# Optimization experiments

Hardware: AMD Instinct MI355X
Metric: run time of the kernel (lower is better)

Reference implementation:

```python
import jax, jax.numpy as jnp
import numpy as np

B, S, D = 2, 2048, 1024  # batch, seq, model_dim
E, K, H = 8, 2, 4096     # experts, top_k, expert hidden
CAP_FACTOR = 1.0


def setup_inputs() -> dict:
    key = jax.random.key(0)
    ks = jax.random.split(key, 6)
    scale_in = 1.0 / np.sqrt(D)
    scale_h = 1.0 / np.sqrt(H)
    return {
        "x": jax.random.normal(ks[0], (B, S, D), jnp.float32),
        "wg": jax.random.normal(ks[1], (D, E), jnp.float32) * scale_in,
        "w1": jax.random.normal(ks[2], (E, D, H), jnp.float32) * scale_in,
        "b1": jnp.zeros((E, H), jnp.float32),
        "w2": jax.random.normal(ks[3], (E, H, D), jnp.float32) * scale_h,
        "b2": jnp.zeros((E, D), jnp.float32),
    }


def _moe_forward(x, wg, w1, b1, w2, b2):
    Bb, Ss, Dd = x.shape
    T = Bb * Ss
    cap = int(K * CAP_FACTOR * ((T + E - 1) // E))  # Tutel capacity rule
    xt = x.reshape(T, Dd)

    # ---- gating ----
    logits = xt @ wg                      # [T, E]
    scores = jax.nn.softmax(logits, axis=-1)
    gates_k, idx_k = jax.lax.top_k(scores, K)  # [T, K]
    # normalize_gate=True: renormalize top-k gates
    gates_k = gates_k / jnp.sum(gates_k, axis=-1, keepdims=True)

    # ---- GShard-style location assignment (slot-major cumsum) ----
    masks = jax.nn.one_hot(idx_k, E, dtype=jnp.int32)           # [T, K, E]
    m = jnp.transpose(masks, (1, 0, 2)).reshape(K * T, E)       # slot-major
    locs_full = jnp.cumsum(m, axis=0) - 1                       # [K*T, E]
    loc = jnp.sum(locs_full * m, axis=-1)                       # [K*T]
    loc = loc.reshape(K, T).T                                   # [T, K]
    valid = (loc < cap).astype(xt.dtype)                        # capacity drop
    loc_c = jnp.clip(loc, 0, cap - 1)

    # ---- dispatch: scatter tokens into [E, cap, D] ----
    contrib = (xt[:, None, :] * valid[:, :, None]).reshape(T * K, Dd)
    disp = jnp.zeros((E, cap, Dd), xt.dtype)
    disp = disp.at[idx_k.reshape(-1), loc_c.reshape(-1)].add(contrib)

    # ---- grouped expert FFN ----
    h = jax.nn.relu(jnp.einsum("ecd,edh->ech", disp, w1) + b1[:, None, :])
    out = jnp.einsum("ech,ehd->ecd", h, w2) + b2[:, None, :]

    # ---- combine (postscore): gather + gate-weighted sum ----
    gathered = out[idx_k, loc_c]                                # [T, K, D]
    y = jnp.einsum("tk,tkd->td", gates_k * valid, gathered)
    return y.reshape(Bb, Ss, Dd)


def reference(x, wg, w1, b1, w2, b2):
    return _moe_forward(x, wg, w1, b1, w2, b2)
```

## Files before the change

kernel.cpp:

```cpp
#include <hip/hip_runtime.h>
#include <stdint.h>

#define NTOK 4096
#define DIM  1024
#define NEXP 8
#define HID  4096
#define CAP  1024

typedef __bf16 bf16x8 __attribute__((ext_vector_type(8)));
typedef float  f32x4  __attribute__((ext_vector_type(4)));

__device__ __forceinline__ unsigned short f2bf(float f) {
  unsigned int u = __float_as_uint(f);
  return (unsigned short)((u + 0x7fffu + ((u >> 16) & 1u)) >> 16);
}

__device__ __forceinline__ float bf2f(unsigned int bits16) {
  return __uint_as_float(bits16 << 16);
}

__device__ __forceinline__ void load_lds16(const void* g, void* l) {
  __builtin_amdgcn_global_load_lds(
      (__attribute__((address_space(1))) void*)g,
      (__attribute__((address_space(3))) void*)l,
      16, 0, 0);
}

__global__ void gating_kernel(const float* __restrict__ x, const float* __restrict__ wg,
                              int* __restrict__ tok_e, float* __restrict__ tok_g) {
  const int t = blockIdx.x;
  const int l = threadIdx.x;
  float acc[NEXP];
#pragma unroll
  for (int e = 0; e < NEXP; ++e) acc[e] = 0.f;

  const float4* x4  = (const float4*)(x + (size_t)t * DIM);
  const float4* wg4 = (const float4*)wg;
#pragma unroll
  for (int i = 0; i < 4; ++i) {
    int dq = i * 64 + l;
    float4 xv = x4[dq];
    float xs[4] = {xv.x, xv.y, xv.z, xv.w};
#pragma unroll
    for (int c = 0; c < 4; ++c) {
      int d = dq * 4 + c;
      float4 wa = wg4[d * 2], wb = wg4[d * 2 + 1];
      acc[0] += xs[c] * wa.x; acc[1] += xs[c] * wa.y;
      acc[2] += xs[c] * wa.z; acc[3] += xs[c] * wa.w;
      acc[4] += xs[c] * wb.x; acc[5] += xs[c] * wb.y;
      acc[6] += xs[c] * wb.z; acc[7] += xs[c] * wb.w;
    }
  }
#pragma unroll
  for (int off = 32; off; off >>= 1)
#pragma unroll
    for (int e = 0; e < NEXP; ++e) acc[e] += __shfl_xor(acc[e], off);

  if (l == 0) {
    float m = acc[0];
#pragma unroll
    for (int e = 1; e < NEXP; ++e) m = fmaxf(m, acc[e]);
    float p[NEXP];
#pragma unroll
    for (int e = 0; e < NEXP; ++e) p[e] = __expf(acc[e] - m);
    int e0 = 0; float b0 = p[0];
#pragma unroll
    for (int e = 1; e < NEXP; ++e) if (p[e] > b0) { b0 = p[e]; e0 = e; }
    int e1 = -1; float b1v = -1.f;
#pragma unroll
    for (int e = 0; e < NEXP; ++e) if (e != e0 && p[e] > b1v) { b1v = p[e]; e1 = e; }
    float inv = 1.f / (b0 + b1v);
    tok_e[2 * t] = e0; tok_e[2 * t + 1] = e1;
    tok_g[2 * t] = b0 * inv; tok_g[2 * t + 1] = b1v * inv;
  }
}

__global__ void scan_kernel(const int* __restrict__ tok_e, int* __restrict__ tok_loc,
                            int* __restrict__ slot_map) {
  const int l = threadIdx.x;
  const unsigned long long below = (1ull << l) - 1ull;
  int base[NEXP];
#pragma unroll
  for (int e = 0; e < NEXP; ++e) base[e] = 0;

  int nxt = tok_e[((0 * 64 + l) & (NTOK - 1)) * 2 + ((0 * 64 + l) >> 12)];
  for (int it = 0; it < 128; ++it) {
    int e = nxt;
    if (it + 1 < 128) {
      int g2 = (it + 1) * 64 + l;
      nxt = tok_e[(g2 & (NTOK - 1)) * 2 + (g2 >> 12)];
    }
    int loc = 0;
#pragma unroll
    for (int ex = 0; ex < NEXP; ++ex) {
      unsigned long long msk = __ballot(e == ex);
      int off = __popcll(msk & below);
      if (e == ex) loc = base[ex] + off;
      base[ex] += __popcll(msk);
    }
    int g = it * 64 + l;
    int k = g >> 12, t = g & (NTOK - 1);
    bool valid = loc < CAP;
    tok_loc[t * 2 + k] = valid ? loc : -1;
    if (valid) slot_map[e * CAP + loc] = t;
  }
#pragma unroll
  for (int ex = 0; ex < NEXP; ++ex) {
    int c = base[ex] < CAP ? base[ex] : CAP;
    for (int i = c + l; i < CAP; i += 64) slot_map[ex * CAP + i] = -1;
  }
}

__global__ void dispatch_kernel(const float* __restrict__ x, const int* __restrict__ slot_map,
                                unsigned short* __restrict__ disp) {
  const int s = blockIdx.x;
  const int tid = threadIdx.x;
  int t = slot_map[s];
  uint2 o;
  if (t >= 0) {
    float4 v = ((const float4*)(x + (size_t)t * DIM))[tid];
    o.x = (unsigned)f2bf(v.x) | ((unsigned)f2bf(v.y) << 16);
    o.y = (unsigned)f2bf(v.z) | ((unsigned)f2bf(v.w) << 16);
  } else {
    o.x = 0u; o.y = 0u;
  }
  ((uint2*)(disp + (size_t)s * DIM))[tid] = o;
}

__global__ void transpose_cvt(const float* __restrict__ in, unsigned short* __restrict__ out,
                              int R, int C) {
  __shared__ float tile[128][65];
  const int e = blockIdx.z;
  const float* inp = in + (size_t)e * R * C;
  unsigned short* outp = out + (size_t)e * R * C;
  const int c0 = blockIdx.x * 64, r0 = blockIdx.y * 128;
  const int t = threadIdx.x;
#pragma unroll
  for (int i = 0; i < 8; ++i) {
    int idx = i * 256 + t;
    int r = idx >> 4, c4 = (idx & 15) * 4;
    float4 v = *(const float4*)(inp + (size_t)(r0 + r) * C + c0 + c4);
    tile[r][c4 + 0] = v.x; tile[r][c4 + 1] = v.y;
    tile[r][c4 + 2] = v.z; tile[r][c4 + 3] = v.w;
  }
  __syncthreads();
#pragma unroll
  for (int i = 0; i < 4; ++i) {
    int idx = i * 256 + t;
    int c = idx >> 4, r8 = (idx & 15) * 8;
    unsigned short s[8];
#pragma unroll
    for (int j = 0; j < 8; ++j) s[j] = f2bf(tile[r8 + j][c]);
    uint4 o;
    o.x = (unsigned)s[0] | ((unsigned)s[1] << 16);
    o.y = (unsigned)s[2] | ((unsigned)s[3] << 16);
    o.z = (unsigned)s[4] | ((unsigned)s[5] << 16);
    o.w = (unsigned)s[6] | ((unsigned)s[7] << 16);
    *(uint4*)(outp + (size_t)(c0 + c) * R + r0 + r8) = o;
  }
}

template <bool RELU>
__global__ __launch_bounds__(256, 4)
void gemm_kernel(const unsigned short* __restrict__ A, const unsigned short* __restrict__ B,
                 const float* __restrict__ bias, unsigned short* __restrict__ C,
                 int N, int K) {
  __shared__ __align__(16) unsigned short As[2][128 * 32];
  __shared__ __align__(16) unsigned short Bs[2][128 * 32];

  int bid = blockIdx.x;
  const int cpx = (int)gridDim.x >> 3;
  bid = (bid & 7) * cpx + (bid >> 3);
  const int ntn = N >> 7;
  const int per_e = 8 * ntn;
  const int e = bid / per_e;
  const int rb = bid - e * per_e;
  const int mtile = rb / ntn;
  const int ntile = rb - mtile * ntn;

  A += (size_t)e * 1024 * K;
  B += (size_t)e * N * K;
  bias += (size_t)e * N;
  C += (size_t)e * 1024 * N;
  const int m0 = mtile * 128;
  const int n0 = ntile * 128;

  const int tid = threadIdx.x;
  const int wave = tid >> 6, lane = tid & 63;
  const int wm = wave >> 1, wn = wave & 1;
  const int quad = lane >> 4;

  const int srow = lane >> 2;
  const int scol = ((lane & 3) ^ (srow & 3)) * 8;
  const unsigned short* gA = A + (size_t)(m0 + wave * 16 + srow) * K + scol;
  const unsigned short* gB = B + (size_t)(n0 + wave * 16 + srow) * K + scol;

  f32x4 acc[4][4] = {};

  const int coff = (quad ^ (lane & 3)) * 8;
  const int arowb = (wm * 64 + (lane & 15)) * 32;
  const int browb = (wn * 64 + (lane & 15)) * 32;

#pragma unroll
  for (int i = 0; i < 2; ++i) {
    load_lds16(gA + (size_t)i * 64 * K, &As[0][(i * 64 + wave * 16) * 32]);
    load_lds16(gB + (size_t)i * 64 * K, &Bs[0][(i * 64 + wave * 16) * 32]);
  }
  gA += 32; gB += 32;

  const int nIter = K >> 5;
  for (int t = 0; t < nIter; ++t) {
    const int cur = t & 1;
    __syncthreads();
    if (t + 1 < nIter) {
#pragma unroll
      for (int i = 0; i < 2; ++i) {
        load_lds16(gA + (size_t)i * 64 * K, &As[cur ^ 1][(i * 64 + wave * 16) * 32]);
        load_lds16(gB + (size_t)i * 64 * K, &Bs[cur ^ 1][(i * 64 + wave * 16) * 32]);
      }
      gA += 32; gB += 32;
    }
    bf16x8 af[4], bfr[4];
#pragma unroll
    for (int i = 0; i < 4; ++i)
      af[i] = *reinterpret_cast<const bf16x8*>(&As[cur][arowb + i * 512 + coff]);
#pragma unroll
    for (int j = 0; j < 4; ++j)
      bfr[j] = *reinterpret_cast<const bf16x8*>(&Bs[cur][browb + j * 512 + coff]);
#pragma unroll
    for (int i = 0; i < 4; ++i)
#pragma unroll
      for (int j = 0; j < 4; ++j)
        acc[i][j] = __builtin_amdgcn_mfma_f32_16x16x32_bf16(af[i], bfr[j], acc[i][j], 0, 0, 0);
  }

  __syncthreads();
  unsigned short* scr = (wave < 2 ? &As[0][0] : &Bs[0][0]) + (wave & 1) * 2304;
  const int lc = lane & 15;
  const int erow = lane >> 3;
  const int ecol = (lane & 7) * 8;
#pragma unroll
  for (int p = 0; p < 2; ++p) {
#pragma unroll
    for (int j = 0; j < 4; ++j) {
      float bj = bias[n0 + wn * 64 + j * 16 + lc];
#pragma unroll
      for (int ii = 0; ii < 2; ++ii) {
#pragma unroll
        for (int rr = 0; rr < 4; ++rr) {
          float v = acc[p * 2 + ii][j][rr] + bj;
          if (RELU) v = fmaxf(v, 0.f);
          scr[(ii * 16 + quad * 4 + rr) * 72 + j * 16 + lc] = f2bf(v);
        }
      }
    }
    __asm__ volatile("s_waitcnt lgkmcnt(0)" ::: "memory");
    unsigned short* Cbase = C + (size_t)(m0 + wm * 64 + p * 32) * N + n0 + wn * 64;
#pragma unroll
    for (int pp = 0; pp < 4; ++pp) {
      uint4 v = *(const uint4*)&scr[(pp * 8 + erow) * 72 + ecol];
      *(uint4*)&Cbase[(size_t)(pp * 8 + erow) * N + ecol] = v;
    }
  }
}

__global__ void combine_kernel(const unsigned short* __restrict__ outb,
                               const int* __restrict__ tok_e, const int* __restrict__ tok_loc,
                               const float* __restrict__ tok_g, float* __restrict__ y) {
  const int t = blockIdx.x;
  const int tid = threadIdx.x;
  int e0 = tok_e[2 * t], e1 = tok_e[2 * t + 1];
  int l0 = tok_loc[2 * t], l1 = tok_loc[2 * t + 1];
  float g0 = tok_g[2 * t], g1 = tok_g[2 * t + 1];
  float ax = 0.f, ay = 0.f, az = 0.f, aw = 0.f;
  if (l0 >= 0) {
    uint2 u = ((const uint2*)(outb + ((size_t)e0 * CAP + l0) * DIM))[tid];
    ax += g0 * bf2f(u.x & 0xffffu); ay += g0 * __uint_as_float(u.x & 0xffff0000u);
    az += g0 * bf2f(u.y & 0xffffu); aw += g0 * __uint_as_float(u.y & 0xffff0000u);
  }
  if (l1 >= 0) {
    uint2 u = ((const uint2*)(outb + ((size_t)e1 * CAP + l1) * DIM))[tid];
    ax += g1 * bf2f(u.x & 0xffffu); ay += g1 * __uint_as_float(u.x & 0xffff0000u);
    az += g1 * bf2f(u.y & 0xffffu); aw += g1 * __uint_as_float(u.y & 0xffff0000u);
  }
  float4 o; o.x = ax; o.y = ay; o.z = az; o.w = aw;
  ((float4*)(y + (size_t)t * DIM))[tid] = o;
}

extern "C" void kernel_launch(void* const* d_in, const int* in_sizes, int n_in,
                              void* d_out, int out_size, void* d_ws, size_t ws_size,
                              hipStream_t stream) {
  const float* x  = (const float*)d_in[0];
  const float* wg = (const float*)d_in[1];
  const float* w1 = (const float*)d_in[2];
  const float* b1 = (const float*)d_in[3];
  const float* w2 = (const float*)d_in[4];
  const float* b2 = (const float*)d_in[5];
  float* y = (float*)d_out;

  char* ws = (char*)d_ws;
  int*   tok_e    = (int*)(ws);
  int*   tok_loc  = (int*)(ws + 32768);
  float* tok_g    = (float*)(ws + 65536);
  int*   slot_map = (int*)(ws + 98304);
  unsigned short* disp = (unsigned short*)(ws + 131072);
  unsigned short* wbuf = (unsigned short*)(ws + 131072 + (16ull << 20));
  unsigned short* h    = (unsigned short*)(ws + 131072 + (80ull << 20));
  unsigned short* outb = (unsigned short*)(ws + 131072 + (144ull << 20));

  gating_kernel<<<NTOK, 64, 0, stream>>>(x, wg, tok_e, tok_g);
  scan_kernel<<<1, 64, 0, stream>>>(tok_e, tok_loc, slot_map);
  dispatch_kernel<<<NEXP * CAP, 256, 0, stream>>>(x, slot_map, disp);
  transpose_cvt<<<dim3(HID / 64, DIM / 128, NEXP), 256, 0, stream>>>(w1, wbuf, DIM, HID);
  gemm_kernel<true><<<NEXP * 8 * (HID / 128), 256, 0, stream>>>(disp, wbuf, b1, h, HID, DIM);
  transpose_cvt<<<dim3(DIM / 64, HID / 128, NEXP), 256, 0, stream>>>(w2, wbuf, HID, DIM);
  gemm_kernel<false><<<NEXP * 8 * (DIM / 128), 256, 0, stream>>>(h, wbuf, b2, outb, DIM, HID);
  combine_kernel<<<NTOK, 256, 0, stream>>>(outb, tok_e, tok_loc, tok_g, y);
}
```

Baseline: 559.2 us.

## Rewrite expert GEMM with 128x256 tiles, 3-stage LDS pipeline, 8 waves

Replaces the 128x128, double-buffered, 4-wave GEMM with a 128x256 tile using 8 waves, a K-step of 64, and a triple-buffered global_load_lds pipeline in 144KB of dynamic LDS. Loads are issued two stages ahead, with explicit vmcnt waits and raw s_barrier instead of __syncthreads. MFMAs run at raised priority. The aim is to hide global load latency and cut barrier and LDS traffic per MFMA. In exchange occupancy drops to one block per CU and the grid gets smaller, which risks tail imbalance, especially on the second GEMM with only 256 blocks.

```diff
diff --git a/kernel.cpp b/kernel.cpp
--- a/kernel.cpp
+++ b/kernel.cpp
@@ -161,17 +161,18 @@
 }
 
 template <bool RELU>
-__global__ __launch_bounds__(256, 4)
-void gemm_kernel(const unsigned short* __restrict__ A, const unsigned short* __restrict__ B,
-                 const float* __restrict__ bias, unsigned short* __restrict__ C,
-                 int N, int K) {
-  __shared__ __align__(16) unsigned short As[2][128 * 32];
-  __shared__ __align__(16) unsigned short Bs[2][128 * 32];
+__global__ __launch_bounds__(512, 1)
+void gemm3(const unsigned short* __restrict__ A, const unsigned short* __restrict__ B,
+           const float* __restrict__ bias, unsigned short* __restrict__ C,
+           int N, int K) {
+  extern __shared__ __align__(16) unsigned short smem[];
+  unsigned short* As = smem;
+  unsigned short* Bs = smem + 3 * 8192;
 
   int bid = blockIdx.x;
   const int cpx = (int)gridDim.x >> 3;
   bid = (bid & 7) * cpx + (bid >> 3);
-  const int ntn = N >> 7;
+  const int ntn = N >> 8;
   const int per_e = 8 * ntn;
   const int e = bid / per_e;
   const int rb = bid - e * per_e;
@@ -183,84 +184,102 @@
   bias += (size_t)e * N;
   C += (size_t)e * 1024 * N;
   const int m0 = mtile * 128;
-  const int n0 = ntile * 128;
+  const int n0 = ntile * 256;
 
   const int tid = threadIdx.x;
-  const int wave = tid >> 6, lane = tid & 63;
-  const int wm = wave >> 1, wn = wave & 1;
+  const int w = tid >> 6, lane = tid & 63;
+  const int wm = w >> 2, wn = w & 3;
   const int quad = lane >> 4;
-
-  const int srow = lane >> 2;
-  const int scol = ((lane & 3) ^ (srow & 3)) * 8;
-  const unsigned short* gA = A + (size_t)(m0 + wave * 16 + srow) * K + scol;
-  const unsigned short* gB = B + (size_t)(n0 + wave * 16 + srow) * K + scol;
+  const int l15 = lane & 15;
+
+  const int srow = lane >> 3;
+  const int scol = ((lane & 7) ^ srow) * 8;
+  const unsigned short* gA = A + (size_t)(m0 + w * 8 + srow) * K + scol;
+  const unsigned short* gB = B + (size_t)(n0 + w * 8 + srow) * K + scol;
+  const int lbase = w * 512;
+
+  int coff[2];
+  coff[0] = ((quad + 0) ^ (lane & 7)) * 8;
+  coff[1] = ((quad + 4) ^ (lane & 7)) * 8;
+  const int arow = (wm * 64 + l15) * 64;
+  const int brow = (wn * 64 + l15) * 64;
 
   f32x4 acc[4][4] = {};
-
-  const int coff = (quad ^ (lane & 3)) * 8;
-  const int arowb = (wm * 64 + (lane & 15)) * 32;
-  const int browb = (wn * 64 + (lane & 15)) * 32;
-
-#pragma unroll
-  for (int i = 0; i < 2; ++i) {
-    load_lds16(gA + (size_t)i * 64 * K, &As[0][(i * 64 + wave * 16) * 32]);
-    load_lds16(gB + (size_t)i * 64 * K, &Bs[0][(i * 64 + wave * 16) * 32]);
-  }
-  gA += 32; gB += 32;
-
-  const int nIter = K >> 5;
-  for (int t = 0; t < nIter; ++t) {
-    const int cur = t & 1;
-    __syncthreads();
-    if (t + 1 < nIter) {
-#pragma unroll
-      for (int i = 0; i < 2; ++i) {
-        load_lds16(gA + (size_t)i * 64 * K, &As[cur ^ 1][(i * 64 + wave * 16) * 32]);
-        load_lds16(gB + (size_t)i * 64 * K, &Bs[cur ^ 1][(i * 64 + wave * 16) * 32]);
+  const int nt = K >> 6;
+
+#define STAGE(T, BUF)                                                           \
+  { _Pragma("unroll")                                                           \
+    for (int q_ = 0; q_ < 2; ++q_)                                              \
+      load_lds16(gA + (size_t)(q_ * 64) * K + (size_t)(T) * 64,                 \
+                 &As[(BUF) * 8192 + lbase + q_ * 4096]);                        \
+    _Pragma("unroll")                                                           \
+    for (int q_ = 0; q_ < 4; ++q_)                                              \
+      load_lds16(gB + (size_t)(q_ * 64) * K + (size_t)(T) * 64,                 \
+                 &Bs[(BUF) * 16384 + lbase + q_ * 4096]); }
+
+  STAGE(0, 0);
+  STAGE(1, 1);
+  asm volatile("s_waitcnt vmcnt(6)" ::: "memory");
+  __builtin_amdgcn_s_barrier();
+  __builtin_amdgcn_sched_barrier(0);
+
+  int cur = 0;
+  for (int t = 0; t < nt; ++t) {
+    const bool s2 = (t + 2) < nt;
+    if (s2) {
+      int nx2 = cur - 1; if (nx2 < 0) nx2 = 2;
+      STAGE(t + 2, nx2);
+    }
+    bf16x8 af[4][2], bfr[4][2];
+#pragma unroll
+    for (int f = 0; f < 4; ++f)
+#pragma unroll
+      for (int kk = 0; kk < 2; ++kk)
+        af[f][kk] = *(const bf16x8*)&As[cur * 8192 + arow + f * 1024 + coff[kk]];
+#pragma unroll
+    for (int j = 0; j < 4; ++j)
+#pragma unroll
+      for (int kk = 0; kk < 2; ++kk)
+        bfr[j][kk] = *(const bf16x8*)&Bs[cur * 16384 + brow + j * 1024 + coff[kk]];
+    __builtin_amdgcn_s_setprio(1);
+#pragma unroll
+    for (int kk = 0; kk < 2; ++kk)
+#pragma unroll
+      for (int i = 0; i < 4; ++i)
+#pragma unroll
+        for (int j = 0; j < 4; ++j)
+          acc[i][j] = __builtin_amdgcn_mfma_f32_16x16x32_bf16(af[i][kk], bfr[j][kk],
+                                                              acc[i][j], 0, 0, 0);
+    __builtin_amdgcn_s_setprio(0);
+    if (s2) { asm volatile("s_waitcnt vmcnt(6)" ::: "memory"); }
+    else    { asm volatile("s_waitcnt vmcnt(0)" ::: "memory"); }
+    __builtin_amdgcn_s_barrier();
+    __builtin_amdgcn_sched_barrier(0);
+    ++cur; if (cur == 3) cur = 0;
+  }
+#undef STAGE
+
+  unsigned short* scr = smem + w * 4608;
+#pragma unroll
+  for (int j = 0; j < 4; ++j) {
+    float bj = bias[n0 + wn * 64 + j * 16 + l15];
+#pragma unroll
+    for (int i = 0; i < 4; ++i)
+#pragma unroll
+      for (int rr = 0; rr < 4; ++rr) {
+        float v = acc[i][j][rr] + bj;
+        if (RELU) v = fmaxf(v, 0.f);
+        scr[(i * 16 + quad * 4 + rr) * 72 + j * 16 + l15] = f2bf(v);
       }
-      gA += 32; gB += 32;
-    }
-    bf16x8 af[4], bfr[4];
-#pragma unroll
-    for (int i = 0; i < 4; ++i)
-      af[i] = *reinterpret_cast<const bf16x8*>(&As[cur][arowb + i * 512 + coff]);
-#pragma unroll
-    for (int j = 0; j < 4; ++j)
-      bfr[j] = *reinterpret_cast<const bf16x8*>(&Bs[cur][browb + j * 512 + coff]);
-#pragma unroll
-    for (int i = 0; i < 4; ++i)
-#pragma unroll
-      for (int j = 0; j < 4; ++j)
-        acc[i][j] = __builtin_amdgcn_mfma_f32_16x16x32_bf16(af[i], bfr[j], acc[i][j], 0, 0, 0);
-  }
-
-  __syncthreads();
-  unsigned short* scr = (wave < 2 ? &As[0][0] : &Bs[0][0]) + (wave & 1) * 2304;
-  const int lc = lane & 15;
+  }
+  __asm__ volatile("s_waitcnt lgkmcnt(0)" ::: "memory");
   const int erow = lane >> 3;
   const int ecol = (lane & 7) * 8;
-#pragma unroll
-  for (int p = 0; p < 2; ++p) {
-#pragma unroll
-    for (int j = 0; j < 4; ++j) {
-      float bj = bias[n0 + wn * 64 + j * 16 + lc];
-#pragma unroll
-      for (int ii = 0; ii < 2; ++ii) {
-#pragma unroll
-        for (int rr = 0; rr < 4; ++rr) {
-          float v = acc[p * 2 + ii][j][rr] + bj;
-          if (RELU) v = fmaxf(v, 0.f);
-          scr[(ii * 16 + quad * 4 + rr) * 72 + j * 16 + lc] = f2bf(v);
-        }
-      }
-    }
-    __asm__ volatile("s_waitcnt lgkmcnt(0)" ::: "memory");
-    unsigned short* Cbase = C + (size_t)(m0 + wm * 64 + p * 32) * N + n0 + wn * 64;
-#pragma unroll
-    for (int pp = 0; pp < 4; ++pp) {
-      uint4 v = *(const uint4*)&scr[(pp * 8 + erow) * 72 + ecol];
-      *(uint4*)&Cbase[(size_t)(pp * 8 + erow) * N + ecol] = v;
-    }
+  unsigned short* Cbase = C + (size_t)(m0 + wm * 64) * N + n0 + wn * 64;
+#pragma unroll
+  for (int p = 0; p < 8; ++p) {
+    uint4 v = *(const uint4*)&scr[(p * 8 + erow) * 72 + ecol];
+    *(uint4*)&Cbase[(size_t)(p * 8 + erow) * N + ecol] = v;
   }
 }
 
@@ -308,12 +327,21 @@
   unsigned short* h    = (unsigned short*)(ws + 131072 + (80ull << 20));
   unsigned short* outb = (unsigned short*)(ws + 131072 + (144ull << 20));
 
+  static int att = 0;
+  if (!att) {
+    (void)hipFuncSetAttribute(reinterpret_cast<const void*>(&gemm3<true>),
+                              hipFuncAttributeMaxDynamicSharedMemorySize, 147456);
+    (void)hipFuncSetAttribute(reinterpret_cast<const void*>(&gemm3<false>),
+                              hipFuncAttributeMaxDynamicSharedMemorySize, 147456);
+    att = 1;
+  }
+
   gating_kernel<<<NTOK, 64, 0, stream>>>(x, wg, tok_e, tok_g);
   scan_kernel<<<1, 64, 0, stream>>>(tok_e, tok_loc, slot_map);
   dispatch_kernel<<<NEXP * CAP, 256, 0, stream>>>(x, slot_map, disp);
   transpose_cvt<<<dim3(HID / 64, DIM / 128, NEXP), 256, 0, stream>>>(w1, wbuf, DIM, HID);
-  gemm_kernel<true><<<NEXP * 8 * (HID / 128), 256, 0, stream>>>(disp, wbuf, b1, h, HID, DIM);
+  gemm3<true><<<NEXP * 8 * (HID / 256), 512, 147456, stream>>>(disp, wbuf, b1, h, HID, DIM);
   transpose_cvt<<<dim3(DIM / 64, HID / 128, NEXP), 256, 0, stream>>>(w2, wbuf, HID, DIM);
-  gemm_kernel<false><<<NEXP * 8 * (DIM / 128), 256, 0, stream>>>(h, wbuf, b2, outb, DIM, HID);
+  gemm3<false><<<NEXP * 8 * (DIM / 256), 512, 147456, stream>>>(h, wbuf, b2, outb, DIM, HID);
   combine_kernel<<<NTOK, 256, 0, stream>>>(outb, tok_e, tok_loc, tok_g, y);
 }
```

New measurement: 516.9 us. -7.6%, faster.
